# Optimization experiments

Hardware: AMD Instinct MI355X
Metric: run time of the kernel (lower is better)

## Reference

```python
import jax, jax.numpy as jnp
import numpy as np

COMMITMENT_COST = 0.25


def setup_inputs() -> dict:
    key = jax.random.key(0)
    k1, k2 = jax.random.split(key)
    inputs = jax.random.normal(k1, (256, 512, 64), dtype=jnp.float32)
    embedding = jax.random.normal(k2, (1024, 64), dtype=jnp.float32) * 4.0
    return {"inputs": inputs, "embedding": embedding}


def reference(inputs, embedding):
    # inputs: [B, T, D], embedding: [K, D]
    input_shape = inputs.shape
    D = embedding.shape[-1]
    flat = inputs.reshape(-1, D)  # [N, D]
    # squared-L2 distances: [N, K]
    distances = (
        jnp.sum(flat * flat, axis=1, keepdims=True)
        + jnp.sum(embedding * embedding, axis=1)[None, :]
        - 2.0 * flat @ embedding.T
    )
    encoding_indices = jnp.argmin(distances, axis=1)  # [N]
    # one-hot @ embedding == gather
    quantized = embedding[encoding_indices].reshape(input_shape)  # [B, T, D]
    # squared-L2 commitment / codebook loss
    e_latent_loss = jnp.sum((jax.lax.stop_gradient(quantized) - inputs) ** 2, axis=-1)
    q_latent_loss = jnp.sum((quantized - jax.lax.stop_gradient(inputs)) ** 2, axis=-1)
    quantization_loss = q_latent_loss + COMMITMENT_COST * e_latent_loss  # [B, T]
    # straight-through estimator
    quantized_sg = inputs + jax.lax.stop_gradient(quantized - inputs)
    encoding_indices = encoding_indices.reshape(input_shape[:-1])  # [B, T]
    return quantized_sg, encoding_indices, quantization_loss
```

## Files before the change

### kernel.cpp

```cpp
#include <hip/hip_runtime.h>
#include <hip/hip_bf16.h>

#define D 64
#define KCODES 1024
#define MARGIN 0.25f
#define OFFSET 2048.0f

typedef __attribute__((ext_vector_type(8))) short bf16x8;
typedef __attribute__((ext_vector_type(4))) float f32x4;

__device__ __forceinline__ unsigned short f2bf(float f) {
    union { __hip_bfloat16 h; unsigned short s; } cv;
    cv.h = __float2bfloat16(f);
    return cv.s;
}
__device__ __forceinline__ float bf2f(unsigned short v) {
    union { unsigned short s; __hip_bfloat16 h; } cv;
    cv.s = v;
    return __bfloat162float(cv.h);
}

__device__ __forceinline__ void stage16(const void* g, void* l) {
    __builtin_amdgcn_global_load_lds(
        (const __attribute__((address_space(1))) void*)g,
        (__attribute__((address_space(3))) void*)l, 16, 0, 0);
}

__global__ __launch_bounds__(256) void prep_kernel(
    const float* __restrict__ emb, float* __restrict__ e2, float* __restrict__ e2b,
    unsigned short* __restrict__ ehi, unsigned short* __restrict__ elo,
    unsigned int* __restrict__ counter) {
    int t = blockIdx.x * 256 + threadIdx.x;
    if (t == 0) *counter = 0u;
    if (t < KCODES) {
        const float4* ep = (const float4*)(emb + (size_t)t * D);
        float s0 = 0.f, s1 = 0.f, s2 = 0.f, s3 = 0.f;
#pragma unroll
        for (int i = 0; i < 16; ++i) {
            float4 v = ep[i];
            s0 = fmaf(v.x, v.x, s0);
            s1 = fmaf(v.y, v.y, s1);
            s2 = fmaf(v.z, v.z, s2);
            s3 = fmaf(v.w, v.w, s3);
        }
        float s = (s0 + s1) + (s2 + s3);
        e2[t] = s;
        e2b[t] = s + OFFSET;
    }
    float v = emb[t];
    unsigned short h = f2bf(v);
    ehi[t] = h;
    elo[t] = f2bf(v - bf2f(h));
}

__global__ __launch_bounds__(256, 4) void vq_mfma_kernel(
    const float* __restrict__ x, const float* __restrict__ emb,
    const float* __restrict__ e2b, const unsigned short* __restrict__ ehi,
    const unsigned short* __restrict__ elo, float* __restrict__ out_q,
    float* __restrict__ out_idx, float* __restrict__ out_loss,
    unsigned int* __restrict__ counter, int* __restrict__ flaglist, int flag_cap) {
    __shared__ float4 lds4[2][512];
    __shared__ int s_bi[128];
    char* ldsc = (char*)&lds4[0][0];
    const int tid = threadIdx.x;
    const int lane = tid & 63;
    const int wave = __builtin_amdgcn_readfirstlane(tid >> 6);
    const int quad = lane >> 4;
    const int l15 = lane & 15;
    const int rowBase = blockIdx.x * 128 + wave * 32;

    bf16x8 ah[2][2], al[2][2];
#pragma unroll
    for (int rs = 0; rs < 2; ++rs) {
        const float* xr = x + (size_t)(rowBase + rs * 16 + l15) * D;
#pragma unroll
        for (int c = 0; c < 2; ++c) {
            const float4* p = (const float4*)(xr + c * 32 + quad * 8);
            float4 f0 = p[0], f1 = p[1];
            float f[8] = {f0.x, f0.y, f0.z, f0.w, f1.x, f1.y, f1.z, f1.w};
            bf16x8 h, l;
#pragma unroll
            for (int j = 0; j < 8; ++j) {
                float v = -2.0f * f[j];
                unsigned short hu = f2bf(v);
                h[j] = (short)hu;
                l[j] = (short)f2bf(v - bf2f(hu));
            }
            ah[rs][c] = h;
            al[rs][c] = l;
        }
    }

    const unsigned short* gs[2];
#pragma unroll
    for (int i = 0; i < 2; ++i) {
        int li = i * 256 + tid;
        int h = li >> 8, row = (li >> 3) & 31, sl = li & 7;
        gs[i] = (h ? elo : ehi) + row * 64 + (sl ^ (row & 7)) * 8;
    }
    char* wbase = ldsc + wave * 1024;

    const int s7 = l15 & 7;
    const int rdA0 = l15 * 128 + ((quad ^ s7) << 4);
    const int rdB0 = l15 * 128 + (((quad + 4) ^ s7) << 4);

    unsigned int m1[2][4], m2[2][4];
#pragma unroll
    for (int rs = 0; rs < 2; ++rs)
#pragma unroll
        for (int r = 0; r < 4; ++r) { m1[rs][r] = 0xFFFFFFFFu; m2[rs][r] = 0xFFFFFFFFu; }

#pragma unroll
    for (int i = 0; i < 2; ++i) stage16(gs[i], wbase + i * 4096);
    float e2v0 = e2b[l15];
    float e2v1 = e2b[16 + l15];
    __syncthreads();

#pragma unroll 1
    for (int g = 0; g < 32; ++g) {
        float e2n0, e2n1;
        if (g < 31) {
            char* wb = wbase + (((g + 1) & 1) << 13);
#pragma unroll
            for (int i = 0; i < 2; ++i)
                stage16(gs[i] + (size_t)(g + 1) * 2048, wb + i * 4096);
            e2n0 = e2b[(g + 1) * 32 + l15];
            e2n1 = e2b[(g + 1) * 32 + 16 + l15];
        }
        __builtin_amdgcn_sched_barrier(0);
        const char* rb = ldsc + ((g & 1) << 13);
#pragma unroll
        for (int tg = 0; tg < 2; ++tg) {
            bf16x8 bh0 = *(const bf16x8*)(rb + tg * 2048 + rdA0);
            bf16x8 bh1 = *(const bf16x8*)(rb + tg * 2048 + rdB0);
            bf16x8 bl0 = *(const bf16x8*)(rb + 4096 + tg * 2048 + rdA0);
            bf16x8 bl1 = *(const bf16x8*)(rb + 4096 + tg * 2048 + rdB0);
            const unsigned tt = (unsigned)(g * 2 + tg);
            const float ev = tg ? e2v1 : e2v0;
            f32x4 c0 = {ev, ev, ev, ev};
#pragma unroll
            for (int rs = 0; rs < 2; ++rs) {
                f32x4 acc = c0;
                acc = __builtin_amdgcn_mfma_f32_16x16x32_bf16(ah[rs][0], bh0, acc, 0, 0, 0);
                acc = __builtin_amdgcn_mfma_f32_16x16x32_bf16(al[rs][0], bh0, acc, 0, 0, 0);
                acc = __builtin_amdgcn_mfma_f32_16x16x32_bf16(ah[rs][0], bl0, acc, 0, 0, 0);
                acc = __builtin_amdgcn_mfma_f32_16x16x32_bf16(ah[rs][1], bh1, acc, 0, 0, 0);
                acc = __builtin_amdgcn_mfma_f32_16x16x32_bf16(al[rs][1], bh1, acc, 0, 0, 0);
                acc = __builtin_amdgcn_mfma_f32_16x16x32_bf16(ah[rs][1], bl1, acc, 0, 0, 0);
#pragma unroll
                for (int r = 0; r < 4; ++r) {
                    unsigned k = (__float_as_uint(acc[r]) & 0xFFFFFFC0u) | tt;
                    unsigned nm2;
                    asm("v_med3_u32 %0, %1, %2, %3"
                        : "=v"(nm2)
                        : "v"(m1[rs][r]), "v"(m2[rs][r]), "v"(k));
                    m2[rs][r] = nm2;
                    m1[rs][r] = (k < m1[rs][r]) ? k : m1[rs][r];
                }
            }
        }
        if (g < 31) { e2v0 = e2n0; e2v1 = e2n1; }
        __syncthreads();
    }

#pragma unroll
    for (int rs = 0; rs < 2; ++rs)
#pragma unroll
        for (int r = 0; r < 4; ++r) {
            unsigned v1 = m1[rs][r], v2 = m2[rs][r];
            const unsigned my1 = v1;
#pragma unroll
            for (int mask = 1; mask < 16; mask <<= 1) {
                unsigned o1 = __shfl_xor(v1, mask);
                unsigned o2 = __shfl_xor(v2, mask);
                unsigned hi = v1 > o1 ? v1 : o1;
                unsigned lo2 = v2 < o2 ? v2 : o2;
                v2 = lo2 < hi ? lo2 : hi;
                v1 = v1 < o1 ? v1 : o1;
            }
            unsigned long long bal = __ballot(my1 == v1);
            int winl = __ffsll((bal >> (quad * 16)) & 0xFFFFull) - 1;
            int code = (int)(v1 & 63u) * 16 + winl;
            if (l15 == 0) {
                int lrow = wave * 32 + rs * 16 + quad * 4 + r;
                s_bi[lrow] = code;
                float f1 = __uint_as_float(v1 & 0xFFFFFFC0u);
                float f2 = __uint_as_float(v2 & 0xFFFFFFC0u);
                if (f2 - f1 < MARGIN) {
                    unsigned slot = atomicAdd(counter, 1u);
                    if (slot < (unsigned)flag_cap) flaglist[slot] = blockIdx.x * 128 + lrow;
                }
            }
        }
    __syncthreads();

    if (tid < 128) {
        const int row = blockIdx.x * 128 + tid;
        const int bi = s_bi[tid];
        const float4* qp = (const float4*)(emb + (size_t)bi * D);
        const float4* xp = (const float4*)(x + (size_t)row * D);
        float4* oq = (float4*)(out_q + (size_t)row * D);
        float l0 = 0.f, l1 = 0.f, l2 = 0.f, l3 = 0.f;
#pragma unroll
        for (int i = 0; i < 16; ++i) {
            float4 q = qp[i];
            float4 xv = xp[i];
            float a0 = q.x - xv.x, a1 = q.y - xv.y, a2 = q.z - xv.z, a3 = q.w - xv.w;
            l0 = fmaf(a0, a0, l0);
            l1 = fmaf(a1, a1, l1);
            l2 = fmaf(a2, a2, l2);
            l3 = fmaf(a3, a3, l3);
            float4 o;
            o.x = xv.x + a0;
            o.y = xv.y + a1;
            o.z = xv.z + a2;
            o.w = xv.w + a3;
            oq[i] = o;
        }
        float s = (l0 + l1) + (l2 + l3);
        out_idx[row] = (float)bi;
        out_loss[row] = s + 0.25f * s;
    }
}

__global__ __launch_bounds__(256) void rescore_kernel(
    const float* __restrict__ x, const float* __restrict__ emb,
    const float* __restrict__ e2, float* __restrict__ out_q,
    float* __restrict__ out_idx, float* __restrict__ out_loss,
    const unsigned int* __restrict__ counter, const int* __restrict__ flaglist,
    int flag_cap) {
    __shared__ float s_x[8][64];
    __shared__ int s_rows[8];
    __shared__ float s_wd[8][4];
    __shared__ int s_wi[8][4];
    __shared__ float s_a[4][64];
    unsigned int n = *counter;
    if (n > (unsigned)flag_cap) n = (unsigned)flag_cap;
    const int tid = threadIdx.x;
    const int lane = tid & 63;
    const int wv = tid >> 6;
    for (unsigned int b = blockIdx.x; b * 8u < n; b += gridDim.x) {
        const unsigned base = b * 8u;
        unsigned nbu = n - base;
        if (nbu > 8u) nbu = 8u;
        const int nb = (int)nbu;
        if (tid < 8) s_rows[tid] = flaglist[base + (tid < nb ? tid : 0)];
        __syncthreads();
        if (tid < 128) {
            int r = tid >> 4, q4 = tid & 15;
            ((float4*)&s_x[r][0])[q4] = ((const float4*)(x + (size_t)s_rows[r] * D))[q4];
        }
        __syncthreads();

        float bd_[8];
        int bi_[8];
#pragma unroll
        for (int r = 0; r < 8; ++r) { bd_[r] = 3.4e38f; bi_[r] = 0; }
#pragma unroll 1
        for (int kk = 0; kk < 4; ++kk) {
            const int k = tid + kk * 256;
            const float4* ekp = (const float4*)(emb + (size_t)k * D);
            float d0[8], d1[8], d2[8], d3[8];
#pragma unroll
            for (int r = 0; r < 8; ++r) { d0[r] = 0.f; d1[r] = 0.f; d2[r] = 0.f; d3[r] = 0.f; }
#pragma unroll 1
            for (int i = 0; i < 16; ++i) {
                float4 ev = ekp[i];
#pragma unroll
                for (int r = 0; r < 8; ++r) {
                    float4 xv = ((const float4*)&s_x[r][0])[i];
                    d0[r] = fmaf(xv.x, ev.x, d0[r]);
                    d1[r] = fmaf(xv.y, ev.y, d1[r]);
                    d2[r] = fmaf(xv.z, ev.z, d2[r]);
                    d3[r] = fmaf(xv.w, ev.w, d3[r]);
                }
            }
            float e2k = e2[k];
#pragma unroll
            for (int r = 0; r < 8; ++r) {
                float dist = fmaf(-2.0f, (d0[r] + d1[r]) + (d2[r] + d3[r]), e2k);
                if (dist < bd_[r]) { bd_[r] = dist; bi_[r] = k; }
            }
        }
#pragma unroll
        for (int r = 0; r < 8; ++r) {
            float v = bd_[r];
            int ix = bi_[r];
#pragma unroll
            for (int mask = 1; mask < 64; mask <<= 1) {
                float ov = __shfl_xor(v, mask);
                int oi = __shfl_xor(ix, mask);
                bool tk = (ov < v) || (ov == v && oi < ix);
                v = tk ? ov : v;
                ix = tk ? oi : ix;
            }
            if (lane == 0) { s_wd[r][wv] = v; s_wi[r][wv] = ix; }
        }
        __syncthreads();
        if (tid < 8) {
            float v = s_wd[tid][0];
            int ix = s_wi[tid][0];
#pragma unroll
            for (int w = 1; w < 4; ++w) {
                float ov = s_wd[tid][w];
                int oi = s_wi[tid][w];
                bool tk = (ov < v) || (ov == v && oi < ix);
                v = tk ? ov : v;
                ix = tk ? oi : ix;
            }
            s_wi[tid][0] = ix;
        }
        __syncthreads();
#pragma unroll
        for (int pass = 0; pass < 2; ++pass) {
            const int rloc = pass * 4 + wv;
            const int row = s_rows[rloc];
            const int fbi = s_wi[rloc][0];
            const float xe = s_x[rloc][lane];
            const float a = emb[(size_t)fbi * D + lane] - xe;
            if (rloc < nb) out_q[(size_t)row * D + lane] = xe + a;
            s_a[wv][lane] = a * a;
            __syncthreads();
            if (lane == 0 && rloc < nb) {
                float l0 = 0.f, l1 = 0.f, l2 = 0.f, l3 = 0.f;
                for (int i2 = 0; i2 < 16; ++i2) {
                    l0 += s_a[wv][4 * i2 + 0];
                    l1 += s_a[wv][4 * i2 + 1];
                    l2 += s_a[wv][4 * i2 + 2];
                    l3 += s_a[wv][4 * i2 + 3];
                }
                float s = (l0 + l1) + (l2 + l3);
                out_loss[row] = s + 0.25f * s;
                out_idx[row] = (float)fbi;
            }
            __syncthreads();
        }
    }
}

extern "C" void kernel_launch(void* const* d_in, const int* in_sizes, int n_in,
                              void* d_out, int out_size, void* d_ws, size_t ws_size,
                              hipStream_t stream) {
    const float* x = (const float*)d_in[0];
    const float* emb = (const float*)d_in[1];
    const int nrows = in_sizes[0] / D;

    float* out_q = (float*)d_out;
    float* out_idx = out_q + (size_t)nrows * D;
    float* out_loss = out_idx + nrows;

    char* ws = (char*)d_ws;
    float* e2 = (float*)ws;
    float* e2b = (float*)(ws + 4096);
    unsigned short* ehi = (unsigned short*)(ws + 8192);
    unsigned short* elo = (unsigned short*)(ws + 8192 + 131072);
    unsigned int* counter = (unsigned int*)(ws + 8192 + 262144);
    int* flaglist = (int*)(ws + 8192 + 262144 + 64);
    long long avail = (long long)ws_size - (8192 + 262144 + 64);
    int flag_cap = (int)(avail / 4);
    if (flag_cap > 16384) flag_cap = 16384;
    if (flag_cap < 1024) flag_cap = 1024;

    prep_kernel<<<(KCODES * D) / 256, 256, 0, stream>>>(emb, e2, e2b, ehi, elo, counter);
    vq_mfma_kernel<<<nrows / 128, 256, 0, stream>>>(x, emb, e2b, ehi, elo, out_q,
                                                    out_idx, out_loss, counter,
                                                    flaglist, flag_cap);
    rescore_kernel<<<1024, 256, 0, stream>>>(x, emb, e2, out_q, out_idx, out_loss,
                                             counter, flaglist, flag_cap);
}
```

Measured before the change: 173.0 us.

## Deepen codebook staging to 4-buffer ring with prefetch distance three

Replaces the double-buffered LDS staging of codebook tiles with a four-slot ring that prefetches three groups ahead, using explicit vmcnt waits plus raw s_barrier in place of a full __syncthreads. The per-code norm table is also staged once into LDS instead of being loaded from global memory every iteration. The aim is to hide global-load latency behind the MFMA work. In exchange the block uses more LDS, which can lower occupancy below the four-blocks launch bound, and the hand-tuned waitcnt counts are fragile.

```diff
diff --git a/kernel.cpp b/kernel.cpp
--- a/kernel.cpp
+++ b/kernel.cpp
@@ -59,7 +59,8 @@
     const unsigned short* __restrict__ elo, float* __restrict__ out_q,
     float* __restrict__ out_idx, float* __restrict__ out_loss,
     unsigned int* __restrict__ counter, int* __restrict__ flaglist, int flag_cap) {
-    __shared__ float4 lds4[2][512];
+    __shared__ float4 lds4[4][512];
+    __shared__ __align__(16) float s_e2b[KCODES];
     __shared__ int s_bi[128];
     char* ldsc = (char*)&lds4[0][0];
     const int tid = threadIdx.x;
@@ -110,25 +111,20 @@
 #pragma unroll
         for (int r = 0; r < 4; ++r) { m1[rs][r] = 0xFFFFFFFFu; m2[rs][r] = 0xFFFFFFFFu; }
 
-#pragma unroll
-    for (int i = 0; i < 2; ++i) stage16(gs[i], wbase + i * 4096);
-    float e2v0 = e2b[l15];
-    float e2v1 = e2b[16 + l15];
-    __syncthreads();
-
-#pragma unroll 1
-    for (int g = 0; g < 32; ++g) {
-        float e2n0, e2n1;
-        if (g < 31) {
-            char* wb = wbase + (((g + 1) & 1) << 13);
-#pragma unroll
-            for (int i = 0; i < 2; ++i)
-                stage16(gs[i] + (size_t)(g + 1) * 2048, wb + i * 4096);
-            e2n0 = e2b[(g + 1) * 32 + l15];
-            e2n1 = e2b[(g + 1) * 32 + 16 + l15];
-        }
-        __builtin_amdgcn_sched_barrier(0);
-        const char* rb = ldsc + ((g & 1) << 13);
+    stage16(e2b + 4 * tid, (char*)s_e2b + wave * 1024);
+#pragma unroll
+    for (int gg = 0; gg < 3; ++gg)
+#pragma unroll
+        for (int i = 0; i < 2; ++i)
+            stage16(gs[i] + (size_t)gg * 2048, wbase + gg * 8192 + i * 4096);
+    asm volatile("s_waitcnt vmcnt(4)" ::: "memory");
+    __builtin_amdgcn_sched_barrier(0);
+    __builtin_amdgcn_s_barrier();
+
+    auto compute_group = [&](int g) {
+        const char* rb = ldsc + (g & 3) * 8192;
+        float e2v0 = s_e2b[g * 32 + l15];
+        float e2v1 = s_e2b[g * 32 + 16 + l15];
 #pragma unroll
         for (int tg = 0; tg < 2; ++tg) {
             bf16x8 bh0 = *(const bf16x8*)(rb + tg * 2048 + rdA0);
@@ -159,9 +155,24 @@
                 }
             }
         }
-        if (g < 31) { e2v0 = e2n0; e2v1 = e2n1; }
-        __syncthreads();
-    }
+    };
+
+#pragma unroll 1
+    for (int g = 0; g < 29; ++g) {
+#pragma unroll
+        for (int i = 0; i < 2; ++i)
+            stage16(gs[i] + (size_t)(g + 3) * 2048, wbase + ((g + 3) & 3) * 8192 + i * 4096);
+        compute_group(g);
+        asm volatile("s_waitcnt vmcnt(4)" ::: "memory");
+        __builtin_amdgcn_sched_barrier(0);
+        __builtin_amdgcn_s_barrier();
+    }
+    compute_group(29);
+    asm volatile("s_waitcnt vmcnt(0)" ::: "memory");
+    __builtin_amdgcn_sched_barrier(0);
+    __builtin_amdgcn_s_barrier();
+    compute_group(30);
+    compute_group(31);
 
 #pragma unroll
     for (int rs = 0; rs < 2; ++rs)
```

After: 170.7 us. Within noise of the previous version (-1.3%).
